# Kernel tuning notes

Measured on AMD Instinct MI355X. Metric: run time of the kernel, lower is better.

Reference implementation:

```python
import jax, jax.numpy as jnp
import numpy as np


def _lsa(cost):
    """Exact rectangular linear sum assignment (Jonker-Volgenant / e-maxx
    Hungarian with potentials). Returns (row_ind, col_ind) matching
    scipy.optimize.linear_sum_assignment (row_ind sorted ascending)."""
    n, m = cost.shape
    transposed = n > m
    if transposed:
        cost = cost.T
        n, m = m, n
    cost = np.asarray(cost, dtype=np.float64)
    INF = 1e18
    u = np.zeros(n + 1)
    v = np.zeros(m + 1)
    p = np.zeros(m + 1, dtype=np.int64)   # p[j]: 1-based row assigned to col j
    way = np.zeros(m + 1, dtype=np.int64)
    for i in range(1, n + 1):
        p[0] = i
        j0 = 0
        minv = np.full(m + 1, INF)
        used = np.zeros(m + 1, dtype=bool)
        while True:
            used[j0] = True
            i0 = p[j0]
            cur = cost[i0 - 1] - u[i0] - v[1:]          # vectorized over cols
            upd = (~used[1:]) & (cur < minv[1:])
            minv[1:] = np.where(upd, cur, minv[1:])
            way[1:] = np.where(upd, j0, way[1:])
            masked = np.where(used[1:], INF, minv[1:])
            j1 = int(np.argmin(masked)) + 1
            delta = masked[j1 - 1]
            u[p[used]] += delta
            v[used] -= delta
            minv[1:] = np.where(used[1:], minv[1:], minv[1:] - delta)
            j0 = j1
            if p[j0] == 0:
                break
        while j0 != 0:
            j1 = way[j0]
            p[j0] = p[j1]
            j0 = j1
    if transposed:
        pairs = sorted((j - 1, p[j] - 1) for j in range(1, m + 1) if p[j] != 0)
    else:
        pairs = sorted((p[j] - 1, j - 1) for j in range(1, m + 1) if p[j] != 0)
    row_ind = np.array([r for r, _ in pairs], dtype=np.int64)
    col_ind = np.array([c for _, c in pairs], dtype=np.int64)
    return row_ind, col_ind


def _row_order(cost_b):
    """Matched rows first (scipy order), then unmatched rows sorted ascending."""
    N = cost_b.shape[0]
    row_ind, _ = _lsa(cost_b)
    remain = sorted(set(range(N)) - set(row_ind.tolist()))
    return np.concatenate([row_ind, np.asarray(remain, dtype=np.int64)])


def _pairwise_l2(seq1, seq2):
    # Fused batched cdist: ||a-b|| = sqrt(|a|^2 + |b|^2 - 2 a.b)
    a2 = jnp.sum(seq1 * seq1, axis=-1)[:, :, None]   # [B,N,1]
    b2 = jnp.sum(seq2 * seq2, axis=-1)[:, None, :]   # [B,1,M]
    ab = jnp.einsum('bnd,bmd->bnm', seq1, seq2)      # [B,N,M]
    return jnp.sqrt(jnp.maximum(a2 + b2 - 2.0 * ab, 0.0))


def setup_inputs() -> dict:
    key = jax.random.key(0)
    k1, k2 = jax.random.split(key)
    B, N, M, D = 16, 512, 448, 1536
    return {
        'seq1': jax.random.normal(k1, (B, N, D), dtype=jnp.float32),
        'seq2': jax.random.normal(k2, (B, M, D), dtype=jnp.float32),
    }


def reference(seq1, seq2):
    cost = np.asarray(_pairwise_l2(seq1, seq2))      # [B,N,M], one fused kernel
    # Hungarian solve is inherently sequential / CPU-bound per batch element.
    perm = np.stack([_row_order(cost[b]) for b in range(cost.shape[0])], 0)
    perm = jnp.asarray(perm)                         # [B,N]
    return jnp.take_along_axis(seq1, perm[:, :, None], axis=1)
```

## Files before the change

### kernel.cpp

```cpp
#include <hip/hip_runtime.h>
#include <math.h>

#define BB 16
#define NN 512
#define MM 448
#define DD 1536

constexpr int TK = 32;

__global__ __launch_bounds__(256) void cost_kernel(const float* __restrict__ s1,
                                                   const float* __restrict__ s2,
                                                   float* __restrict__ Ct) {
  __shared__ float As[TK][68];
  __shared__ float Bs[TK][68];
  const int b = blockIdx.z;
  const int ibase = blockIdx.x * 64;
  const int jbase = blockIdx.y * 64;
  const int tid = threadIdx.x;
  const float* s1b = s1 + ((size_t)b * NN + ibase) * DD;
  const float* s2b = s2 + ((size_t)b * MM + jbase) * DD;
  const int ix = (tid & 15) * 4;
  const int jy = (tid >> 4) * 4;
  double acc[16];
#pragma unroll
  for (int t = 0; t < 16; ++t) acc[t] = 0.0;

  for (int k0 = 0; k0 < DD; k0 += TK) {
#pragma unroll
    for (int rep = 0; rep < 2; ++rep) {
      int idx = tid + rep * 256;
      int r = idx >> 3;
      int c4 = (idx & 7) * 4;
      float4 a = *(const float4*)(s1b + (size_t)r * DD + k0 + c4);
      As[c4 + 0][r] = a.x; As[c4 + 1][r] = a.y; As[c4 + 2][r] = a.z; As[c4 + 3][r] = a.w;
      float4 bb = *(const float4*)(s2b + (size_t)r * DD + k0 + c4);
      Bs[c4 + 0][r] = bb.x; Bs[c4 + 1][r] = bb.y; Bs[c4 + 2][r] = bb.z; Bs[c4 + 3][r] = bb.w;
    }
    __syncthreads();
    float pacc[16];
#pragma unroll
    for (int t = 0; t < 16; ++t) pacc[t] = 0.f;
#pragma unroll 8
    for (int kk = 0; kk < TK; ++kk) {
      float4 av = *(const float4*)&As[kk][ix];
      float4 bv = *(const float4*)&Bs[kk][jy];
      float a[4] = {av.x, av.y, av.z, av.w};
      float bq[4] = {bv.x, bv.y, bv.z, bv.w};
#pragma unroll
      for (int t = 0; t < 4; ++t)
#pragma unroll
        for (int q = 0; q < 4; ++q) {
          float d = a[t] - bq[q];
          pacc[t * 4 + q] = fmaf(d, d, pacc[t * 4 + q]);
        }
    }
#pragma unroll
    for (int t = 0; t < 16; ++t) acc[t] += (double)pacc[t];
    __syncthreads();
  }
#pragma unroll
  for (int t = 0; t < 4; ++t)
#pragma unroll
    for (int q = 0; q < 4; ++q) {
      int i = ibase + ix + t;
      int jj = jbase + jy + q;
      float d2 = (float)acc[t * 4 + q];
      Ct[((size_t)b * MM + jj) * NN + i] = sqrtf(fmaxf(d2, 0.f));
    }
}

__device__ __forceinline__ unsigned wave_min_bcast_u32(unsigned x) {
  int v = (int)x;
#define ST(C) { int o = __builtin_amdgcn_update_dpp(-1, v, C, 0xF, 0xF, false); \
                v = ((unsigned)o < (unsigned)v) ? o : v; }
  ST(0x111) ST(0x112) ST(0x114) ST(0x118) ST(0x142) ST(0x143)
#undef ST
  return (unsigned)__builtin_amdgcn_readlane(v, 63);
}

__device__ __forceinline__ double wave_min_bcast_f64_fast(double x) {
  union DU { double d; unsigned u[2]; };
  DU v; v.d = x;
  unsigned hmin = wave_min_bcast_u32(v.u[1]);
  unsigned lc = (v.u[1] == hmin) ? v.u[0] : 0xFFFFFFFFu;
  unsigned lmin = wave_min_bcast_u32(lc);
  DU r; r.u[0] = lmin; r.u[1] = hmin;
  return r.d;
}

__device__ __forceinline__ float wave_min_bcast_f32(float x) {
  union FU { float f; int i; };
  FU v; v.f = x;
  const int INFB = 0x7f7fffff;
#define DPP1(CTRL) { FU o; \
  o.i = __builtin_amdgcn_update_dpp(INFB, v.i, CTRL, 0xF, 0xF, false); \
  if (o.f < v.f) v.f = o.f; }
  DPP1(0x111) DPP1(0x112) DPP1(0x114) DPP1(0x118) DPP1(0x142) DPP1(0x143)
#undef DPP1
  FU r; r.i = __builtin_amdgcn_readlane(v.i, 63);
  return r.f;
}

__global__ __launch_bounds__(64) void jv_kernel(const float* __restrict__ Ct,
                                                int* __restrict__ perm) {
  const int b = blockIdx.x;
  const float* C = Ct + (size_t)b * MM * NN;
  __shared__ double u_lds[MM + 1];
  __shared__ int p_lds[NN + 1];
  __shared__ int way_lds[NN + 1];
  __shared__ int colOwner[NN];
  __shared__ int rowMatched[MM];
  __shared__ int freeL[MM];
  __shared__ int nfree_s;
  __shared__ int cnt_lds[64];
  const int lane = threadIdx.x;
  const int jbase = 8 * lane + 1;

  if (lane == 0) u_lds[0] = 0.0;
  for (int t = lane; t <= NN; t += 64) { p_lds[t] = 0; way_lds[t] = 0; }
  for (int t = lane; t < NN; t += 64) colOwner[t] = -1;
  for (int t = lane; t < MM; t += 64) rowMatched[t] = 0;
  asm volatile("s_waitcnt lgkmcnt(0)" ::: "memory");

  {
    const float4* r40 = (const float4*)(C);
    const float4* r41 = (const float4*)(C + (size_t)NN);
    float4 ca = r40[2 * lane], cb = r40[2 * lane + 1];
    float4 na = r41[2 * lane], nb = r41[2 * lane + 1];
    for (int r = 0; r < MM; ++r) {
      int rp = (r + 2 < MM) ? (r + 2) : (MM - 1);
      const float4* r4n = (const float4*)(C + (size_t)rp * NN);
      float4 pa = r4n[2 * lane], pb = r4n[2 * lane + 1];
      float c[8] = {ca.x, ca.y, ca.z, ca.w, cb.x, cb.y, cb.z, cb.w};
      float lm = 1e30f; int la = 0;
#pragma unroll
      for (int q = 0; q < 8; ++q)
        if (c[q] < lm) { lm = c[q]; la = 8 * lane + q; }
      float rm = wave_min_bcast_f32(lm);
      unsigned long long bm = __ballot(lm == rm);
      int sl = (int)__ffsll((unsigned long long)bm) - 1;
      int jc = __builtin_amdgcn_readlane(la, sl);
      if (lane == 0) {
        u_lds[r + 1] = (double)rm;
        if (colOwner[jc] < 0) {
          colOwner[jc] = r;
          rowMatched[r] = 1;
          p_lds[jc + 1] = r + 1;
        }
      }
      ca = na; cb = nb; na = pa; nb = pb;
    }
  }
  double vcol[8];
#pragma unroll
  for (int q = 0; q < 8; ++q) vcol[q] = 0.0;
  asm volatile("s_waitcnt lgkmcnt(0)" ::: "memory");

  if (lane == 0) {
    int n = 0;
    for (int r = 0; r < MM; ++r) if (!rowMatched[r]) freeL[n++] = r;
    nfree_s = n;
  }
  asm volatile("s_waitcnt lgkmcnt(0)" ::: "memory");
  int nfree = nfree_s;

  for (int pass = 0; pass < 2; ++pass) {
    int prev = nfree; nfree = 0; int k = 0;
    if (prev == 0) continue;
    int i = freeL[0];
    {
      const float4* r4p = (const float4*)(C + (size_t)i * NN);
      float4 ca = r4p[2 * lane];
      float4 cb = r4p[2 * lane + 1];
      while (true) {
        const int kn = k + 1;
        const int ig = (kn < prev) ? freeL[kn] : 0;
        const float4* r4n = (const float4*)(C + (size_t)ig * NN);
        float4 nca = r4n[2 * lane];
        float4 ncb = r4n[2 * lane + 1];

        float c[8] = {ca.x, ca.y, ca.z, ca.w, cb.x, cb.y, cb.z, cb.w};
        double m1 = 1e18, m2 = 1e18; int a1 = 0;
#pragma unroll
        for (int q = 0; q < 8; ++q) {
          double h = (double)c[q] - vcol[q];
          if (h < m1) { m2 = m1; m1 = h; a1 = 8 * lane + q; }
          else if (h < m2) m2 = h;
        }
        double umin = wave_min_bcast_f64_fast(m1);
        unsigned long long bm = __ballot(m1 == umin);
        int sl = (int)__ffsll((unsigned long long)bm) - 1;
        int j1 = __builtin_amdgcn_readlane(a1, sl);
        double cd = (lane == sl) ? m2 : m1;
        double usub = wave_min_bcast_f64_fast(cd);
        const bool strict = (umin < usub);
        if (strict && (j1 >> 3) == lane) {
          double dec = usub - umin;
#pragma unroll
          for (int qq = 0; qq < 8; ++qq) if (qq == (j1 & 7)) vcol[qq] -= dec;
        }
        const int powner = p_lds[j1 + 1];
        asm volatile("" ::: "memory");
        const int i0 = powner - 1;
        if (lane == 0) { u_lds[i + 1] = usub; p_lds[j1 + 1] = i + 1; }
        const bool reproc = (i0 >= 0) && strict;
        if (i0 >= 0 && !strict) {
          if (lane == 0) freeL[nfree] = i0;
          nfree++;
        }
        asm volatile("s_waitcnt lgkmcnt(0)" ::: "memory");
        if (reproc) {
          i = i0;
          const float4* r4m = (const float4*)(C + (size_t)i * NN);
          ca = r4m[2 * lane];
          cb = r4m[2 * lane + 1];
        } else {
          k = kn;
          if (k >= prev) break;
          i = ig; ca = nca; cb = ncb;
        }
      }
    }
  }

  const int nf3 = nfree;
  for (int fi = 0; fi < nf3; ++fi) {
    const int i = freeL[fi] + 1;
    if (lane == 0) p_lds[0] = i;
    double minv[8], rec[8];
    int preg[8], wayr[8];
#pragma unroll
    for (int q = 0; q < 8; ++q) { minv[q] = 1e18; rec[q] = 0.0; preg[q] = 0; wayr[q] = 0; }
    int usedm = 0;
    double cum = 0.0;
    int j0 = 0, i0 = i;
    asm volatile("s_waitcnt lgkmcnt(0)" ::: "memory");

    const float4* r4p = (const float4*)(C + (size_t)(i0 - 1) * NN);
    float4 ca = r4p[2 * lane];
    float4 cb = r4p[2 * lane + 1];
    double uu = u_lds[i0];

    while (true) {
      float c[8] = {ca.x, ca.y, ca.z, ca.w, cb.x, cb.y, cb.z, cb.w};
#pragma unroll
      for (int q = 0; q < 8; ++q) {
        if (!((usedm >> q) & 1)) {
          double cur = ((double)c[q] - uu) - vcol[q];
          cur = (cur > 0.0) ? cur : 0.0;
          if (cur < minv[q]) { minv[q] = cur; wayr[q] = j0; }
        }
      }
      double m01 = (minv[1] < minv[0]) ? minv[1] : minv[0];
      int    a01 = (minv[1] < minv[0]) ? jbase + 1 : jbase + 0;
      double m23 = (minv[3] < minv[2]) ? minv[3] : minv[2];
      int    a23 = (minv[3] < minv[2]) ? jbase + 3 : jbase + 2;
      double m45 = (minv[5] < minv[4]) ? minv[5] : minv[4];
      int    a45 = (minv[5] < minv[4]) ? jbase + 5 : jbase + 4;
      double m67 = (minv[7] < minv[6]) ? minv[7] : minv[6];
      int    a67 = (minv[7] < minv[6]) ? jbase + 7 : jbase + 6;
      double m03 = (m23 < m01) ? m23 : m01;
      int    a03 = (m23 < m01) ? a23 : a01;
      double m47 = (m67 < m45) ? m67 : m45;
      int    a47 = (m67 < m45) ? a67 : a45;
      double lm = (m47 < m03) ? m47 : m03;
      int    la = (m47 < m03) ? a47 : a03;

      int pcand = p_lds[la];

      float lmf = (float)lm;
      float rmf = wave_min_bcast_f32(lmf);
      unsigned long long bmf = __ballot(lmf == rmf);
      int slf = (int)__ffsll(bmf) - 1;
      int pnf = __builtin_amdgcn_readlane(pcand, slf);
      int rs = (pnf > 0) ? (pnf - 1) : 0;
      const float4* r4s = (const float4*)(C + (size_t)rs * NN);
      float4 sca = r4s[2 * lane];
      float4 scb = r4s[2 * lane + 1];
      double uus = u_lds[pnf];

      union DU { double d; unsigned u[2]; };
      DU lv; lv.d = lm;
      unsigned hmin = wave_min_bcast_u32(lv.u[1]);
      unsigned lc = (lv.u[1] == hmin) ? lv.u[0] : 0xFFFFFFFFu;
      unsigned lmin = wave_min_bcast_u32(lc);
      unsigned long long bm = __ballot((lv.u[1] == hmin) && (lv.u[0] == lmin));
      int sl = (int)__ffsll((unsigned long long)bm) - 1;
      int j1 = __builtin_amdgcn_readlane(la, sl);
      int pn = __builtin_amdgcn_readlane(pcand, sl);
      DU dd; dd.u[0] = lmin; dd.u[1] = hmin;
      double delta = dd.d;
      cum += delta;
#pragma unroll
      for (int q = 0; q < 8; ++q) minv[q] -= delta;
      j0 = j1;
      if (pn == 0) break;
#pragma unroll
      for (int q = 0; q < 8; ++q)
        if (j1 == jbase + q) {
          usedm |= (1 << q); preg[q] = pn; rec[q] = cum; minv[q] = 1e18;
        }
      i0 = pn;
      if (pn == pnf) {
        ca = sca; cb = scb; uu = uus;
      } else {
        const float4* r4m = (const float4*)(C + (size_t)(pn - 1) * NN);
        ca = r4m[2 * lane];
        cb = r4m[2 * lane + 1];
        uu = u_lds[pn];
      }
    }

    if (lane == 0) u_lds[i] += cum;
#pragma unroll
    for (int q = 0; q < 8; ++q) {
      way_lds[jbase + q] = wayr[q];
      if ((usedm >> q) & 1) {
        double d = cum - rec[q];
        vcol[q] -= d;
        u_lds[preg[q]] += d;
      }
    }
    asm volatile("s_waitcnt lgkmcnt(0)" ::: "memory");
    if (lane == 0) {
      int jj = j0;
      while (jj != 0) { int jp = way_lds[jj]; p_lds[jj] = p_lds[jp]; jj = jp; }
    }
    asm volatile("s_waitcnt lgkmcnt(0)" ::: "memory");
  }

  int mask = 0, cnt = 0;
#pragma unroll
  for (int q = 0; q < 8; ++q)
    if (p_lds[jbase + q] != 0) { mask |= 1 << q; cnt++; }
  cnt_lds[lane] = cnt;
  asm volatile("s_waitcnt lgkmcnt(0)" ::: "memory");
  int pre = 0;
  for (int l = 0; l < 64; ++l) { int cl = cnt_lds[l]; if (l < lane) pre += cl; }
  int mpos = pre;
  int upos = MM + (8 * lane - pre);
#pragma unroll
  for (int q = 0; q < 8; ++q) {
    int col = 8 * lane + q;
    if ((mask >> q) & 1) perm[b * NN + mpos++] = col;
    else                 perm[b * NN + upos++] = col;
  }
}

__global__ __launch_bounds__(256) void gather_kernel(const float* __restrict__ s1,
                                                     const int* __restrict__ perm,
                                                     float* __restrict__ out) {
  const int bi = blockIdx.x;
  const int b = bi >> 9;
  const int src = perm[bi];
  const float4* sp = (const float4*)(s1 + ((size_t)b * NN + src) * DD);
  float4* dp = (float4*)(out + (size_t)bi * DD);
  for (int t = threadIdx.x; t < DD / 4; t += 256) dp[t] = sp[t];
}

extern "C" void kernel_launch(void* const* d_in, const int* in_sizes, int n_in,
                              void* d_out, int out_size, void* d_ws, size_t ws_size,
                              hipStream_t stream) {
  const float* s1 = (const float*)d_in[0];
  const float* s2 = (const float*)d_in[1];
  float* out = (float*)d_out;
  float* Ct = (float*)d_out;
  int* perm = (int*)d_ws;

  dim3 cg(NN / 64, MM / 64, BB);
  cost_kernel<<<cg, 256, 0, stream>>>(s1, s2, Ct);
  jv_kernel<<<BB, 64, 0, stream>>>(Ct, perm);
  gather_kernel<<<BB * NN, 256, 0, stream>>>(s1, perm, out);
}
```

Before: 6.409 ms.

## Restructure JV augmenting loop with fast float wave-min and branchless used-column masking

Replaces the double-precision two-pass wave minimum with a float DPP minimum that falls back to the exact two-pass u32 path only when several lanes tie, and uses it in both the auction passes and the Dijkstra augmentation. Used columns are now excluded by adding a large offset (coff) instead of a per-column bitmask branch, and column owners are kept in registers (pm) so the p_lds lookup inside the loop goes away. Per-column rec/preg values move to LDS, and the auction-style pre-pass runs four times instead of twice. These changes aim to shorten the serial per-iteration latency of the assignment loop. In exchange the speculative next-row prefetch is dropped, and the stale pm snapshot and float tie detection need care to keep results exact.

```diff
diff --git a/kernel.cpp b/kernel.cpp
--- a/kernel.cpp
+++ b/kernel.cpp
@@ -78,16 +78,6 @@
   return (unsigned)__builtin_amdgcn_readlane(v, 63);
 }
 
-__device__ __forceinline__ double wave_min_bcast_f64_fast(double x) {
-  union DU { double d; unsigned u[2]; };
-  DU v; v.d = x;
-  unsigned hmin = wave_min_bcast_u32(v.u[1]);
-  unsigned lc = (v.u[1] == hmin) ? v.u[0] : 0xFFFFFFFFu;
-  unsigned lmin = wave_min_bcast_u32(lc);
-  DU r; r.u[0] = lmin; r.u[1] = hmin;
-  return r.d;
-}
-
 __device__ __forceinline__ float wave_min_bcast_f32(float x) {
   union FU { float f; int i; };
   FU v; v.f = x;
@@ -101,6 +91,34 @@
   return r.f;
 }
 
+__device__ __forceinline__ double readlane_f64(double x, int sl) {
+  union { double d; int i[2]; } v, r;
+  v.d = x;
+  r.i[0] = __builtin_amdgcn_readlane(v.i[0], sl);
+  r.i[1] = __builtin_amdgcn_readlane(v.i[1], sl);
+  return r.d;
+}
+
+__device__ __forceinline__ void exact_min_sl(double x, double& mn, int& sl) {
+  float xf = (float)x;
+  float rf = wave_min_bcast_f32(xf);
+  unsigned long long bm = __ballot(xf == rf);
+  if (__popcll(bm) == 1) {
+    sl = (int)__ffsll(bm) - 1;
+    mn = readlane_f64(x, sl);
+  } else {
+    union { double d; unsigned u[2]; } v, r;
+    v.d = x;
+    unsigned hmin = wave_min_bcast_u32(v.u[1]);
+    unsigned lc = (v.u[1] == hmin) ? v.u[0] : 0xFFFFFFFFu;
+    unsigned lmin = wave_min_bcast_u32(lc);
+    unsigned long long b2 = __ballot((v.u[1] == hmin) && (v.u[0] == lmin));
+    sl = (int)__ffsll(b2) - 1;
+    r.u[0] = lmin; r.u[1] = hmin;
+    mn = r.d;
+  }
+}
+
 __global__ __launch_bounds__(64) void jv_kernel(const float* __restrict__ Ct,
                                                 int* __restrict__ perm) {
   const int b = blockIdx.x;
@@ -108,6 +126,8 @@
   __shared__ double u_lds[MM + 1];
   __shared__ int p_lds[NN + 1];
   __shared__ int way_lds[NN + 1];
+  __shared__ double rec_lds[NN + 1];
+  __shared__ int preg_lds[NN + 1];
   __shared__ int colOwner[NN];
   __shared__ int rowMatched[MM];
   __shared__ int freeL[MM];
@@ -164,7 +184,7 @@
   asm volatile("s_waitcnt lgkmcnt(0)" ::: "memory");
   int nfree = nfree_s;
 
-  for (int pass = 0; pass < 2; ++pass) {
+  for (int pass = 0; pass < 4; ++pass) {
     int prev = nfree; nfree = 0; int k = 0;
     if (prev == 0) continue;
     int i = freeL[0];
@@ -187,12 +207,12 @@
           if (h < m1) { m2 = m1; m1 = h; a1 = 8 * lane + q; }
           else if (h < m2) m2 = h;
         }
-        double umin = wave_min_bcast_f64_fast(m1);
-        unsigned long long bm = __ballot(m1 == umin);
-        int sl = (int)__ffsll((unsigned long long)bm) - 1;
+        double umin; int sl;
+        exact_min_sl(m1, umin, sl);
         int j1 = __builtin_amdgcn_readlane(a1, sl);
         double cd = (lane == sl) ? m2 : m1;
-        double usub = wave_min_bcast_f64_fast(cd);
+        double usub; int sl2;
+        exact_min_sl(cd, usub, sl2);
         const bool strict = (umin < usub);
         if (strict && (j1 >> 3) == lane) {
           double dec = usub - umin;
@@ -227,98 +247,91 @@
   for (int fi = 0; fi < nf3; ++fi) {
     const int i = freeL[fi] + 1;
     if (lane == 0) p_lds[0] = i;
-    double minv[8], rec[8];
-    int preg[8], wayr[8];
-#pragma unroll
-    for (int q = 0; q < 8; ++q) { minv[q] = 1e18; rec[q] = 0.0; preg[q] = 0; wayr[q] = 0; }
-    int usedm = 0;
+    double minv[8], coff[8];
+    int wayr[8], pm[8];
+#pragma unroll
+    for (int q = 0; q < 8; ++q) { minv[q] = 1e18; coff[q] = 0.0; wayr[q] = 0; }
+#pragma unroll
+    for (int q = 0; q < 8; ++q) pm[q] = p_lds[jbase + q];
     double cum = 0.0;
-    int j0 = 0, i0 = i;
+    int j0 = 0;
     asm volatile("s_waitcnt lgkmcnt(0)" ::: "memory");
 
-    const float4* r4p = (const float4*)(C + (size_t)(i0 - 1) * NN);
-    float4 ca = r4p[2 * lane];
-    float4 cb = r4p[2 * lane + 1];
-    double uu = u_lds[i0];
+    const float4* r4p = (const float4*)(C + (size_t)(i - 1) * NN);
+    float4 na = r4p[2 * lane];
+    float4 nb = r4p[2 * lane + 1];
+    double uu = u_lds[i];
 
     while (true) {
-      float c[8] = {ca.x, ca.y, ca.z, ca.w, cb.x, cb.y, cb.z, cb.w};
+      float c8[8] = {na.x, na.y, na.z, na.w, nb.x, nb.y, nb.z, nb.w};
 #pragma unroll
       for (int q = 0; q < 8; ++q) {
-        if (!((usedm >> q) & 1)) {
-          double cur = ((double)c[q] - uu) - vcol[q];
-          cur = (cur > 0.0) ? cur : 0.0;
-          if (cur < minv[q]) { minv[q] = cur; wayr[q] = j0; }
-        }
+        double cur = (((double)c8[q] - uu) - vcol[q]) + coff[q];
+        cur = (cur > 0.0) ? cur : 0.0;
+        bool imp = cur < minv[q];
+        minv[q] = imp ? cur : minv[q];
+        wayr[q] = imp ? j0 : wayr[q];
       }
       double m01 = (minv[1] < minv[0]) ? minv[1] : minv[0];
       int    a01 = (minv[1] < minv[0]) ? jbase + 1 : jbase + 0;
+      int    p01 = (minv[1] < minv[0]) ? pm[1] : pm[0];
       double m23 = (minv[3] < minv[2]) ? minv[3] : minv[2];
       int    a23 = (minv[3] < minv[2]) ? jbase + 3 : jbase + 2;
+      int    p23 = (minv[3] < minv[2]) ? pm[3] : pm[2];
       double m45 = (minv[5] < minv[4]) ? minv[5] : minv[4];
       int    a45 = (minv[5] < minv[4]) ? jbase + 5 : jbase + 4;
+      int    p45 = (minv[5] < minv[4]) ? pm[5] : pm[4];
       double m67 = (minv[7] < minv[6]) ? minv[7] : minv[6];
       int    a67 = (minv[7] < minv[6]) ? jbase + 7 : jbase + 6;
+      int    p67 = (minv[7] < minv[6]) ? pm[7] : pm[6];
       double m03 = (m23 < m01) ? m23 : m01;
       int    a03 = (m23 < m01) ? a23 : a01;
+      int    p03 = (m23 < m01) ? p23 : p01;
       double m47 = (m67 < m45) ? m67 : m45;
       int    a47 = (m67 < m45) ? a67 : a45;
+      int    p47 = (m67 < m45) ? p67 : p45;
       double lm = (m47 < m03) ? m47 : m03;
       int    la = (m47 < m03) ? a47 : a03;
-
-      int pcand = p_lds[la];
-
-      float lmf = (float)lm;
-      float rmf = wave_min_bcast_f32(lmf);
-      unsigned long long bmf = __ballot(lmf == rmf);
-      int slf = (int)__ffsll(bmf) - 1;
-      int pnf = __builtin_amdgcn_readlane(pcand, slf);
-      int rs = (pnf > 0) ? (pnf - 1) : 0;
-      const float4* r4s = (const float4*)(C + (size_t)rs * NN);
-      float4 sca = r4s[2 * lane];
-      float4 scb = r4s[2 * lane + 1];
-      double uus = u_lds[pnf];
-
-      union DU { double d; unsigned u[2]; };
-      DU lv; lv.d = lm;
-      unsigned hmin = wave_min_bcast_u32(lv.u[1]);
-      unsigned lc = (lv.u[1] == hmin) ? lv.u[0] : 0xFFFFFFFFu;
-      unsigned lmin = wave_min_bcast_u32(lc);
-      unsigned long long bm = __ballot((lv.u[1] == hmin) && (lv.u[0] == lmin));
-      int sl = (int)__ffsll((unsigned long long)bm) - 1;
+      int    lp = (m47 < m03) ? p47 : p03;
+
+      double delta; int sl;
+      exact_min_sl(lm, delta, sl);
       int j1 = __builtin_amdgcn_readlane(la, sl);
-      int pn = __builtin_amdgcn_readlane(pcand, sl);
-      DU dd; dd.u[0] = lmin; dd.u[1] = hmin;
-      double delta = dd.d;
+      int pn = __builtin_amdgcn_readlane(lp, sl);
       cum += delta;
 #pragma unroll
       for (int q = 0; q < 8; ++q) minv[q] -= delta;
       j0 = j1;
       if (pn == 0) break;
-#pragma unroll
-      for (int q = 0; q < 8; ++q)
-        if (j1 == jbase + q) {
-          usedm |= (1 << q); preg[q] = pn; rec[q] = cum; minv[q] = 1e18;
-        }
-      i0 = pn;
-      if (pn == pnf) {
-        ca = sca; cb = scb; uu = uus;
-      } else {
-        const float4* r4m = (const float4*)(C + (size_t)(pn - 1) * NN);
-        ca = r4m[2 * lane];
-        cb = r4m[2 * lane + 1];
-        uu = u_lds[pn];
+
+      const float4* r4m = (const float4*)(C + (size_t)(pn - 1) * NN);
+      na = r4m[2 * lane];
+      nb = r4m[2 * lane + 1];
+      uu = u_lds[pn];
+
+      {
+        const int ow = (j1 - 1) >> 3;
+        const int qs = (j1 - 1) & 7;
+#pragma unroll
+        for (int q = 0; q < 8; ++q) if (qs == q) {
+          bool me = (lane == ow);
+          minv[q] = me ? 5e17 : minv[q];
+          coff[q] = me ? 1e18 : coff[q];
+        }
+        if (lane == 0) { rec_lds[j1] = cum; preg_lds[j1] = pn; }
       }
     }
 
     if (lane == 0) u_lds[i] += cum;
+    asm volatile("s_waitcnt lgkmcnt(0)" ::: "memory");
 #pragma unroll
     for (int q = 0; q < 8; ++q) {
       way_lds[jbase + q] = wayr[q];
-      if ((usedm >> q) & 1) {
-        double d = cum - rec[q];
+      if (coff[q] != 0.0) {
+        double d = cum - rec_lds[jbase + q];
+        int pr = preg_lds[jbase + q];
         vcol[q] -= d;
-        u_lds[preg[q]] += d;
+        u_lds[pr] += d;
       }
     }
     asm volatile("s_waitcnt lgkmcnt(0)" ::: "memory");
```

Result: slower. 7.001 ms (+9.2%).
